# Performance work log

Hardware: AMD Instinct MI355X
Metric: run time of the kernel (lower is better)

Reference implementation:

```python
import jax, jax.numpy as jnp
import numpy as np

DIM = 768
HEADS = 12
HEAD_DIM = DIM // HEADS
HIDDEN = 4 * DIM
B, N = 32, 577
EPS = 1e-5


def _layernorm(x, g, b):
    mu = jnp.mean(x, axis=-1, keepdims=True)
    var = jnp.mean(jnp.square(x - mu), axis=-1, keepdims=True)
    return (x - mu) * jax.lax.rsqrt(var + EPS) * g + b


def setup_inputs() -> dict:
    key = jax.random.key(0)
    ks = jax.random.split(key, 8)
    s = lambda fan_in: 1.0 / np.sqrt(fan_in)
    return {
        "x": jax.random.normal(ks[0], (B, N, DIM), jnp.float32),
        "cp_mask": jax.random.uniform(ks[1], (1, 1, N, N), jnp.float32),
        "ln1_g": jnp.ones((DIM,), jnp.float32),
        "ln1_b": jnp.zeros((DIM,), jnp.float32),
        "w_qkv": jax.random.uniform(ks[2], (DIM, 3 * DIM), jnp.float32, -s(DIM), s(DIM)),
        "w_proj": jax.random.uniform(ks[3], (DIM, DIM), jnp.float32, -s(DIM), s(DIM)),
        "b_proj": jnp.zeros((DIM,), jnp.float32),
        "ln2_g": jnp.ones((DIM,), jnp.float32),
        "ln2_b": jnp.zeros((DIM,), jnp.float32),
        "w_fc1": jax.random.uniform(ks[4], (DIM, HIDDEN), jnp.float32, -s(DIM), s(DIM)),
        "b_fc1": jnp.zeros((HIDDEN,), jnp.float32),
        "w_fc2": jax.random.uniform(ks[5], (HIDDEN, DIM), jnp.float32, -s(HIDDEN), s(HIDDEN)),
        "b_fc2": jnp.zeros((DIM,), jnp.float32),
    }


def reference(x, cp_mask, ln1_g, ln1_b, w_qkv, w_proj, b_proj,
              ln2_g, ln2_b, w_fc1, b_fc1, w_fc2, b_fc2):
    scale = HEAD_DIM ** -0.5
    # --- attention branch ---
    h = _layernorm(x, ln1_g, ln1_b)
    qkv = (h @ w_qkv).reshape(B, N, 3, HEADS, HEAD_DIM)
    q, k, v = jnp.moveaxis(qkv, 2, 0)            # each [B,N,H,Dh]
    q = q.transpose(0, 2, 1, 3)                   # [B,H,N,Dh]
    k = k.transpose(0, 2, 1, 3)
    v = v.transpose(0, 2, 1, 3)
    attn = jnp.einsum('bhnd,bhmd->bhnm', q, k) * scale * cp_mask
    attn = jax.nn.softmax(attn, axis=-1)
    out = jnp.einsum('bhnm,bhmd->bhnd', attn, v)
    out = out.transpose(0, 2, 1, 3).reshape(B, N, DIM)
    out = out @ w_proj + b_proj
    x = x + out
    # --- MLP branch ---
    h = _layernorm(x, ln2_g, ln2_b)
    h = jax.nn.gelu(h @ w_fc1 + b_fc1, approximate=False)
    h = h @ w_fc2 + b_fc2
    return x + h
```

## Files before the change

### kernel.cpp

```cpp
#include <hip/hip_runtime.h>
#include <math.h>

typedef unsigned short u16;
typedef unsigned int u32;
typedef __attribute__((ext_vector_type(8))) short bf16x8;
typedef __attribute__((ext_vector_type(4))) float f32x4;

#define B_    32
#define N_    577
#define DIM_  768
#define HEADS_ 12
#define HD_   64
#define HID_  3072
#define MTOT_ (B_*N_)
#define NP_   640

__device__ __forceinline__ u16 f2b(float f){
  u32 u = __builtin_bit_cast(u32, f);
  u += 0x7fffu + ((u >> 16) & 1u);
  return (u16)(u >> 16);
}
__device__ __forceinline__ u32 cvtpk(float lo, float hi){
  u32 r;
  asm("v_cvt_pk_bf16_f32 %0, %1, %2" : "=v"(r) : "v"(lo), "v"(hi));
  return r;
}

__device__ __forceinline__ void gl_lds16(const void* g, void* l){
  __builtin_amdgcn_global_load_lds(
      (const __attribute__((address_space(1))) u32*)g,
      (__attribute__((address_space(3))) u32*)l, 16, 0, 0);
}
__device__ __forceinline__ void gl_lds4(const void* g, void* l){
  __builtin_amdgcn_global_load_lds(
      (const __attribute__((address_space(1))) u32*)g,
      (__attribute__((address_space(3))) u32*)l, 4, 0, 0);
}

__global__ __launch_bounds__(256) void convT(const float* __restrict__ w,
                                             u16* __restrict__ wt, int K, int N){
  __shared__ float t[32][33];
  int n0 = blockIdx.x * 32, k0 = blockIdx.y * 32;
  int tx = threadIdx.x, ty = threadIdx.y;
  #pragma unroll
  for (int j = 0; j < 4; ++j)
    t[ty + j*8][tx] = w[(size_t)(k0 + ty + j*8) * N + n0 + tx];
  __syncthreads();
  #pragma unroll
  for (int j = 0; j < 4; ++j)
    wt[(size_t)(n0 + ty + j*8) * K + k0 + tx] = f2b(t[tx][ty + j*8]);
}

__global__ __launch_bounds__(256) void ln_k(const float* __restrict__ x,
                                            const float* __restrict__ g,
                                            const float* __restrict__ b,
                                            u16* __restrict__ out){
  int row = blockIdx.x, tid = threadIdx.x;
  const float* xr = x + (size_t)row * DIM_;
  float v0 = xr[tid], v1 = xr[tid + 256], v2 = xr[tid + 512];
  float s = v0 + v1 + v2;
  float s2 = v0*v0 + v1*v1 + v2*v2;
  #pragma unroll
  for (int m = 1; m < 64; m <<= 1){ s += __shfl_xor(s, m); s2 += __shfl_xor(s2, m); }
  __shared__ float ws[8];
  int wid = tid >> 6, ln = tid & 63;
  if (ln == 0){ ws[wid] = s; ws[4 + wid] = s2; }
  __syncthreads();
  s  = ws[0] + ws[1] + ws[2] + ws[3];
  s2 = ws[4] + ws[5] + ws[6] + ws[7];
  float mu = s * (1.0f / DIM_);
  float var = s2 * (1.0f / DIM_) - mu * mu;
  float rs = rsqrtf(var + 1e-5f);
  u16* orow = out + (size_t)row * DIM_;
  orow[tid]       = f2b((v0 - mu) * rs * g[tid]       + b[tid]);
  orow[tid + 256] = f2b((v1 - mu) * rs * g[tid + 256] + b[tid + 256]);
  orow[tid + 512] = f2b((v2 - mu) * rs * g[tid + 512] + b[tid + 512]);
}

#define BM 128
#define BN 128
#define BK 32

template<int EPI>
__global__ __launch_bounds__(256) void gemm_bt(
    const u16* __restrict__ A, const u16* __restrict__ Bt,
    int M, int N, int K,
    const float* __restrict__ bias,
    const float* __restrict__ resid,
    float* __restrict__ outf,
    u16* __restrict__ outb,
    u16* __restrict__ qb, u16* __restrict__ kb, u16* __restrict__ vtb)
{
  __shared__ u16 Al[BM * BK];
  __shared__ u16 Bl[BN * BK];
  int tid = threadIdx.x;
  int wid = tid >> 6, l = tid & 63, ln = l & 15, sub = l >> 4;
  int wm = wid >> 1, wn = wid & 1;

  int nwg  = gridDim.x * gridDim.y;
  int flat = blockIdx.x + gridDim.x * blockIdx.y;
  int q8 = nwg >> 3, r8 = nwg & 7;
  int xcd = flat & 7, j8 = flat >> 3;
  int wgid = (xcd < r8 ? xcd * (q8 + 1) : r8 * (q8 + 1) + (xcd - r8) * q8) + j8;
  int tm = wgid / gridDim.y;
  int tn = wgid - tm * gridDim.y;

  f32x4 acc[4][4] = {};
  int arow = tid >> 2;
  int acol = (tid & 3) * 8;

  int gr0 = tm * BM + arow;      if (gr0 >= M) gr0 = M - 1;
  int gr1 = tm * BM + arow + 64; if (gr1 >= M) gr1 = M - 1;
  const u16* ga0 = A + (size_t)gr0 * K + acol;
  const u16* ga1 = A + (size_t)gr1 * K + acol;
  const u16* gb0 = Bt + (size_t)(tn * BN + arow) * K + acol;
  const u16* gb1 = Bt + (size_t)(tn * BN + arow + 64) * K + acol;
  u16* la0 = &Al[arow * BK + acol];
  u16* la1 = &Al[(arow + 64) * BK + acol];
  u16* lb0 = &Bl[arow * BK + acol];
  u16* lb1 = &Bl[(arow + 64) * BK + acol];

  const int ktiles = K / BK;
  for (int kt = 0; kt < ktiles; ++kt){
    int kbase = kt * BK;
    gl_lds16(ga0 + kbase, la0);
    gl_lds16(ga1 + kbase, la1);
    gl_lds16(gb0 + kbase, lb0);
    gl_lds16(gb1 + kbase, lb1);
    __syncthreads();
    bf16x8 af[4], bfr[4];
    #pragma unroll
    for (int mi = 0; mi < 4; ++mi) af[mi]  = *(const bf16x8*)&Al[(wm*64 + mi*16 + ln) * BK + sub*8];
    #pragma unroll
    for (int ni = 0; ni < 4; ++ni) bfr[ni] = *(const bf16x8*)&Bl[(wn*64 + ni*16 + ln) * BK + sub*8];
    #pragma unroll
    for (int mi = 0; mi < 4; ++mi)
      #pragma unroll
      for (int ni = 0; ni < 4; ++ni)
        acc[mi][ni] = __builtin_amdgcn_mfma_f32_16x16x32_bf16(af[mi], bfr[ni], acc[mi][ni], 0, 0, 0);
    __syncthreads();
  }

  #pragma unroll
  for (int mi = 0; mi < 4; ++mi){
    int rbase = tm * BM + wm * 64 + mi * 16 + sub * 4;
    #pragma unroll
    for (int ni = 0; ni < 4; ++ni){
      int col = tn * BN + wn * 64 + ni * 16 + ln;
      #pragma unroll
      for (int r = 0; r < 4; ++r){
        int grow = rbase + r;
        if (grow >= M) continue;
        float val = acc[mi][ni][r];
        if (EPI == 0){
          u32 bb = (u32)grow / 577u;
          u32 nn = (u32)grow - bb * 577u;
          int which = col / 768;
          int rem = col - which * 768;
          int hh = rem >> 6;
          int d  = col & 63;
          if (which == 0)
            qb[(((size_t)bb * HEADS_ + hh) * N_ + nn) * HD_ + d] = f2b(val);
          else if (which == 1)
            kb[(((size_t)bb * HEADS_ + hh) * N_ + nn) * HD_ + d] = f2b(val);
          else
            vtb[(((size_t)bb * HEADS_ + hh) * HD_ + d) * NP_ + nn] = f2b(val);
        } else if (EPI == 1){
          outf[(size_t)grow * N + col] = val + bias[col] + resid[(size_t)grow * N + col];
        } else {
          float t = val + bias[col];
          float ge = 0.5f * t * (1.0f + erff(t * 0.70710678118654752f));
          outb[(size_t)grow * N + col] = f2b(ge);
        }
      }
    }
  }
}

__global__ __launch_bounds__(256) void attn_k(
    const u16* __restrict__ q, const u16* __restrict__ k,
    const u16* __restrict__ vt, const float* __restrict__ mask,
    u16* __restrict__ o)
{
  const float SCALE = 0.125f;
  int bh = blockIdx.x, qt = blockIdx.y;
  int tid = threadIdx.x;
  int wid = tid >> 6, l = tid & 63, ln = l & 15, sub = l >> 4;
  int b = bh / HEADS_, hh = bh - b * HEADS_;
  int qrow0_blk = qt * 64;
  int qrow0 = qrow0_blk + wid * 16;

  __shared__ u16 Kl[64 * 64];
  __shared__ u16 Vl[64 * 64];
  __shared__ float Ml[64 * 64];
  __shared__ u16 Pl[4][16 * 64];

  int qr = qrow0 + ln; if (qr > N_ - 1) qr = N_ - 1;
  const u16* qbase = q + ((size_t)bh * N_ + qr) * HD_;
  bf16x8 qf0 = *(const bf16x8*)&qbase[sub * 8];
  bf16x8 qf1 = *(const bf16x8*)&qbase[32 + sub * 8];

  f32x4 oacc[4] = {};
  float mrun = -1e30f, lrun = 0.f;

  for (int mt = 0; mt < 10; ++mt){
    int mbase = mt * 64;
    #pragma unroll
    for (int p = 0; p < 2; ++p){
      int row = (tid >> 3) + p * 32;
      int sc = (tid & 7) ^ (row & 7);
      int kr = mbase + row; if (kr > N_ - 1) kr = N_ - 1;
      gl_lds16(&k[((size_t)bh * N_ + kr) * HD_ + sc * 8], &Kl[row * 64 + (tid & 7) * 8]);
      gl_lds16(&vt[((size_t)bh * HD_ + row) * NP_ + mbase + sc * 8], &Vl[row * 64 + (tid & 7) * 8]);
    }
    if (mbase + 63 < N_){
      #pragma unroll
      for (int p = 0; p < 4; ++p){
        int row = (tid >> 4) + p * 16;
        int grow = qrow0_blk + row; if (grow > N_ - 1) grow = N_ - 1;
        int sc = (tid & 15) ^ (row & 15);
        gl_lds16(&mask[(size_t)grow * N_ + mbase + sc * 4], &Ml[row * 64 + (tid & 15) * 4]);
      }
    } else {
      #pragma unroll
      for (int p = 0; p < 16; ++p){
        int row = (tid >> 6) + p * 4;
        int grow = qrow0_blk + row; if (grow > N_ - 1) grow = N_ - 1;
        int kp = tid & 63;
        int lcol = ((((kp >> 2) ^ (row & 15)) << 2) | (kp & 3));
        int gcol = mbase + lcol; if (gcol > N_ - 1) gcol = N_ - 1;
        gl_lds4(&mask[(size_t)grow * N_ + gcol], &Ml[row * 64 + kp]);
      }
    }
    __syncthreads();

    f32x4 s[4];
    #pragma unroll
    for (int c = 0; c < 4; ++c){
      int krow = c * 16 + ln;
      bf16x8 kf0 = *(const bf16x8*)&Kl[krow * 64 + ((sub    ) ^ (krow & 7)) * 8];
      bf16x8 kf1 = *(const bf16x8*)&Kl[krow * 64 + ((4 + sub) ^ (krow & 7)) * 8];
      f32x4 z = {};
      z = __builtin_amdgcn_mfma_f32_16x16x32_bf16(kf0, qf0, z, 0, 0, 0);
      z = __builtin_amdgcn_mfma_f32_16x16x32_bf16(kf1, qf1, z, 0, 0, 0);
      s[c] = z;
    }
    int mrow = wid * 16 + ln;
    #pragma unroll
    for (int c = 0; c < 4; ++c){
      f32x4 mv = *(const f32x4*)&Ml[mrow * 64 + (((c * 4 + sub) ^ ln) << 2)];
      int mg0 = mbase + c * 16 + sub * 4;
      #pragma unroll
      for (int r = 0; r < 4; ++r){
        if (mg0 + r < N_) s[c][r] = s[c][r] * SCALE * mv[r];
        else              s[c][r] = -1e30f;
      }
    }
    float pm = s[0][0];
    #pragma unroll
    for (int c = 0; c < 4; ++c)
      #pragma unroll
      for (int r = 0; r < 4; ++r) pm = fmaxf(pm, s[c][r]);
    pm = fmaxf(pm, __shfl_xor(pm, 16));
    pm = fmaxf(pm, __shfl_xor(pm, 32));
    float mnew = fmaxf(mrun, pm);
    float alpha = __expf(mrun - mnew);
    mrun = mnew;
    float ps = 0.f;
    #pragma unroll
    for (int c = 0; c < 4; ++c)
      #pragma unroll
      for (int r = 0; r < 4; ++r){
        float p = __expf(s[c][r] - mrun);
        s[c][r] = p;
        ps += p;
      }
    ps += __shfl_xor(ps, 16);
    ps += __shfl_xor(ps, 32);
    lrun = lrun * alpha + ps;
    #pragma unroll
    for (int c = 0; c < 4; ++c)
      #pragma unroll
      for (int h = 0; h < 2; ++h){
        int kk = c * 16 + sub * 4 + 2 * h;
        u32 w = cvtpk(s[c][2 * h], s[c][2 * h + 1]);
        *(u32*)&Pl[wid][ln * 64 + (((kk >> 3) ^ (ln & 7)) << 3) + (kk & 7)] = w;
      }
    float a_d[4];
    #pragma unroll
    for (int r = 0; r < 4; ++r) a_d[r] = __shfl(alpha, sub * 4 + r);
    #pragma unroll
    for (int dt = 0; dt < 4; ++dt)
      #pragma unroll
      for (int r = 0; r < 4; ++r) oacc[dt][r] *= a_d[r];
    #pragma unroll
    for (int kbv = 0; kbv < 2; ++kbv){
      bf16x8 pa = *(const bf16x8*)&Pl[wid][ln * 64 + (((kbv * 4 + sub) ^ (ln & 7)) << 3)];
      #pragma unroll
      for (int dt = 0; dt < 4; ++dt){
        int vrow = dt * 16 + ln;
        bf16x8 vf = *(const bf16x8*)&Vl[vrow * 64 + (((kbv * 4 + sub) ^ (vrow & 7)) << 3)];
        oacc[dt] = __builtin_amdgcn_mfma_f32_16x16x32_bf16(pa, vf, oacc[dt], 0, 0, 0);
      }
    }
    __syncthreads();
  }
  float rinv = 1.0f / lrun;
  float inv_d[4];
  #pragma unroll
  for (int r = 0; r < 4; ++r) inv_d[r] = __shfl(rinv, sub * 4 + r);
  #pragma unroll
  for (int dt = 0; dt < 4; ++dt)
    #pragma unroll
    for (int r = 0; r < 4; ++r){
      int qg = qrow0 + sub * 4 + r;
      if (qg < N_)
        o[((size_t)b * N_ + qg) * DIM_ + hh * HD_ + dt * 16 + ln] = f2b(oacc[dt][r] * inv_d[r]);
    }
}

#define OFF_WQKV  0ull
#define OFF_WPROJ 3538944ull
#define OFF_WFC1  4718592ull
#define OFF_WFC2  9437184ull
#define OFF_BUFA  14155776ull
#define OFF_BUFB  (OFF_BUFA + 28360704ull)
#define OFF_BUFC  (OFF_BUFB + 28360704ull)
#define OFF_VT    (OFF_BUFC + 28360704ull)

extern "C" void kernel_launch(void* const* d_in, const int* in_sizes, int n_in,
                              void* d_out, int out_size, void* d_ws, size_t ws_size,
                              hipStream_t stream)
{
  const float* x     = (const float*)d_in[0];
  const float* mask  = (const float*)d_in[1];
  const float* ln1g  = (const float*)d_in[2];
  const float* ln1b  = (const float*)d_in[3];
  const float* wqkv  = (const float*)d_in[4];
  const float* wproj = (const float*)d_in[5];
  const float* bproj = (const float*)d_in[6];
  const float* ln2g  = (const float*)d_in[7];
  const float* ln2b  = (const float*)d_in[8];
  const float* wfc1  = (const float*)d_in[9];
  const float* bfc1  = (const float*)d_in[10];
  const float* wfc2  = (const float*)d_in[11];
  const float* bfc2  = (const float*)d_in[12];
  float* out = (float*)d_out;

  char* ws = (char*)d_ws;
  u16* wqkv_t  = (u16*)(ws + OFF_WQKV);
  u16* wproj_t = (u16*)(ws + OFF_WPROJ);
  u16* wfc1_t  = (u16*)(ws + OFF_WFC1);
  u16* wfc2_t  = (u16*)(ws + OFF_WFC2);
  u16* hbuf  = (u16*)(ws + OFF_BUFA);
  u16* obuf  = (u16*)(ws + OFF_BUFA);
  u16* qbuf  = (u16*)(ws + OFF_BUFB);
  u16* h2buf = (u16*)(ws + OFF_BUFB);
  u16* kbuf  = (u16*)(ws + OFF_BUFC);
  u16* vtbuf = (u16*)(ws + OFF_VT);
  u16* h3buf = (u16*)(ws + OFF_BUFC);

  dim3 tb(32, 8);
  convT<<<dim3(2304/32, 768/32), tb, 0, stream>>>(wqkv,  wqkv_t,  768,  2304);
  convT<<<dim3(768/32,  768/32), tb, 0, stream>>>(wproj, wproj_t, 768,  768);
  convT<<<dim3(3072/32, 768/32), tb, 0, stream>>>(wfc1,  wfc1_t,  768,  3072);
  convT<<<dim3(768/32, 3072/32), tb, 0, stream>>>(wfc2,  wfc2_t,  3072, 768);

  ln_k<<<MTOT_, 256, 0, stream>>>(x, ln1g, ln1b, hbuf);

  gemm_bt<0><<<dim3(145, 18), 256, 0, stream>>>(hbuf, wqkv_t, MTOT_, 2304, 768,
      nullptr, nullptr, nullptr, nullptr, qbuf, kbuf, vtbuf);

  attn_k<<<dim3(384, 10), 256, 0, stream>>>(qbuf, kbuf, vtbuf, mask, obuf);

  gemm_bt<1><<<dim3(145, 6), 256, 0, stream>>>(obuf, wproj_t, MTOT_, 768, 768,
      bproj, x, out, nullptr, nullptr, nullptr, nullptr);

  ln_k<<<MTOT_, 256, 0, stream>>>(out, ln2g, ln2b, h2buf);

  const int M0 = 9216, M1 = MTOT_ - M0;
  gemm_bt<2><<<dim3(72, 24), 256, 0, stream>>>(h2buf, wfc1_t, M0, 3072, 768,
      bfc1, nullptr, nullptr, h3buf, nullptr, nullptr, nullptr);
  gemm_bt<1><<<dim3(72, 6), 256, 0, stream>>>(h3buf, wfc2_t, M0, 768, 3072,
      bfc2, out, out, nullptr, nullptr, nullptr, nullptr);
  gemm_bt<2><<<dim3(73, 24), 256, 0, stream>>>(h2buf + (size_t)M0 * 768, wfc1_t, M1, 3072, 768,
      bfc1, nullptr, nullptr, h3buf, nullptr, nullptr, nullptr);
  gemm_bt<1><<<dim3(73, 6), 256, 0, stream>>>(h3buf, wfc2_t, M1, 768, 3072,
      bfc2, out + (size_t)M0 * 768, out + (size_t)M0 * 768, nullptr, nullptr, nullptr, nullptr);
}
```

Measured before the change: 908.0 us.

## Double-buffer LDS tiles in GEMM to overlap global loads with MFMA

The GEMM kernel now keeps two LDS buffers for the A and B tiles. It preloads the first k-tile, then issues the direct-to-LDS loads for the next k-tile before running the MFMAs on the current one. This hides global-memory latency behind compute and removes one barrier per k-iteration. In exchange, LDS use per workgroup doubles, which may lower occupancy.

Result: faster. 868.1 us (-4.4%).

```diff
diff --git a/kernel.cpp b/kernel.cpp
--- a/kernel.cpp
+++ b/kernel.cpp
@@ -91,8 +91,8 @@
     u16* __restrict__ outb,
     u16* __restrict__ qb, u16* __restrict__ kb, u16* __restrict__ vtb)
 {
-  __shared__ u16 Al[BM * BK];
-  __shared__ u16 Bl[BN * BK];
+  __shared__ u16 Al[2][BM * BK];
+  __shared__ u16 Bl[2][BN * BK];
   int tid = threadIdx.x;
   int wid = tid >> 6, l = tid & 63, ln = l & 15, sub = l >> 4;
   int wm = wid >> 1, wn = wid & 1;
@@ -115,30 +115,38 @@
   const u16* ga1 = A + (size_t)gr1 * K + acol;
   const u16* gb0 = Bt + (size_t)(tn * BN + arow) * K + acol;
   const u16* gb1 = Bt + (size_t)(tn * BN + arow + 64) * K + acol;
-  u16* la0 = &Al[arow * BK + acol];
-  u16* la1 = &Al[(arow + 64) * BK + acol];
-  u16* lb0 = &Bl[arow * BK + acol];
-  u16* lb1 = &Bl[(arow + 64) * BK + acol];
+  int s0 = arow * BK + acol;
+  int s1 = (arow + 64) * BK + acol;
 
   const int ktiles = K / BK;
+  gl_lds16(ga0, &Al[0][s0]);
+  gl_lds16(ga1, &Al[0][s1]);
+  gl_lds16(gb0, &Bl[0][s0]);
+  gl_lds16(gb1, &Bl[0][s1]);
+  __syncthreads();
+
+  int cur = 0;
   for (int kt = 0; kt < ktiles; ++kt){
-    int kbase = kt * BK;
-    gl_lds16(ga0 + kbase, la0);
-    gl_lds16(ga1 + kbase, la1);
-    gl_lds16(gb0 + kbase, lb0);
-    gl_lds16(gb1 + kbase, lb1);
-    __syncthreads();
+    int nxt = cur ^ 1;
+    if (kt + 1 < ktiles){
+      int kb = (kt + 1) * BK;
+      gl_lds16(ga0 + kb, &Al[nxt][s0]);
+      gl_lds16(ga1 + kb, &Al[nxt][s1]);
+      gl_lds16(gb0 + kb, &Bl[nxt][s0]);
+      gl_lds16(gb1 + kb, &Bl[nxt][s1]);
+    }
     bf16x8 af[4], bfr[4];
     #pragma unroll
-    for (int mi = 0; mi < 4; ++mi) af[mi]  = *(const bf16x8*)&Al[(wm*64 + mi*16 + ln) * BK + sub*8];
-    #pragma unroll
-    for (int ni = 0; ni < 4; ++ni) bfr[ni] = *(const bf16x8*)&Bl[(wn*64 + ni*16 + ln) * BK + sub*8];
+    for (int mi = 0; mi < 4; ++mi) af[mi]  = *(const bf16x8*)&Al[cur][(wm*64 + mi*16 + ln) * BK + sub*8];
+    #pragma unroll
+    for (int ni = 0; ni < 4; ++ni) bfr[ni] = *(const bf16x8*)&Bl[cur][(wn*64 + ni*16 + ln) * BK + sub*8];
     #pragma unroll
     for (int mi = 0; mi < 4; ++mi)
       #pragma unroll
       for (int ni = 0; ni < 4; ++ni)
         acc[mi][ni] = __builtin_amdgcn_mfma_f32_16x16x32_bf16(af[mi], bfr[ni], acc[mi][ni], 0, 0, 0);
     __syncthreads();
+    cur = nxt;
   }
 
   #pragma unroll
```

## Triple-buffer GEMM LDS tiles with async prefetch and XOR-swizzled layout

Applied to the files above, without the earlier changes.

Converts the GEMM main loop to a three-stage LDS ring buffer. Global-to-LDS loads are issued two tiles ahead, and explicit vmcnt waits plus a single barrier per iteration replace the two syncthreads. It also XOR-swizzles the k-column chunk by row, so fragment reads from LDS avoid bank conflicts. This uses three times the LDS per block, which may reduce occupancy, and it relies on careful waitcnt accounting for correctness.

Measured after the change: 869.3 us. 4.3% less time.

```diff
diff --git a/kernel.cpp b/kernel.cpp
--- a/kernel.cpp
+++ b/kernel.cpp
@@ -91,8 +91,8 @@
     u16* __restrict__ outb,
     u16* __restrict__ qb, u16* __restrict__ kb, u16* __restrict__ vtb)
 {
-  __shared__ u16 Al[BM * BK];
-  __shared__ u16 Bl[BN * BK];
+  __shared__ u16 Al[3][BM * BK];
+  __shared__ u16 Bl[3][BN * BK];
   int tid = threadIdx.x;
   int wid = tid >> 6, l = tid & 63, ln = l & 15, sub = l >> 4;
   int wm = wid >> 1, wn = wid & 1;
@@ -107,38 +107,53 @@
 
   f32x4 acc[4][4] = {};
   int arow = tid >> 2;
-  int acol = (tid & 3) * 8;
+  int t4   = tid & 3;
+  int scol = (t4 ^ ((arow >> 1) & 3)) * 8;
 
   int gr0 = tm * BM + arow;      if (gr0 >= M) gr0 = M - 1;
   int gr1 = tm * BM + arow + 64; if (gr1 >= M) gr1 = M - 1;
-  const u16* ga0 = A + (size_t)gr0 * K + acol;
-  const u16* ga1 = A + (size_t)gr1 * K + acol;
-  const u16* gb0 = Bt + (size_t)(tn * BN + arow) * K + acol;
-  const u16* gb1 = Bt + (size_t)(tn * BN + arow + 64) * K + acol;
-  u16* la0 = &Al[arow * BK + acol];
-  u16* la1 = &Al[(arow + 64) * BK + acol];
-  u16* lb0 = &Bl[arow * BK + acol];
-  u16* lb1 = &Bl[(arow + 64) * BK + acol];
+  const u16* ga0 = A + (size_t)gr0 * K + scol;
+  const u16* ga1 = A + (size_t)gr1 * K + scol;
+  const u16* gb0 = Bt + (size_t)(tn * BN + arow) * K + scol;
+  const u16* gb1 = Bt + (size_t)(tn * BN + arow + 64) * K + scol;
+  int s0 = arow * BK + t4 * 8;
+  int s1 = (arow + 64) * BK + t4 * 8;
+  int csw = (sub ^ ((ln >> 1) & 3)) * 8;
 
   const int ktiles = K / BK;
+  gl_lds16(ga0,      &Al[0][s0]);
+  gl_lds16(ga1,      &Al[0][s1]);
+  gl_lds16(gb0,      &Bl[0][s0]);
+  gl_lds16(gb1,      &Bl[0][s1]);
+  gl_lds16(ga0 + BK, &Al[1][s0]);
+  gl_lds16(ga1 + BK, &Al[1][s1]);
+  gl_lds16(gb0 + BK, &Bl[1][s0]);
+  gl_lds16(gb1 + BK, &Bl[1][s1]);
+
   for (int kt = 0; kt < ktiles; ++kt){
-    int kbase = kt * BK;
-    gl_lds16(ga0 + kbase, la0);
-    gl_lds16(ga1 + kbase, la1);
-    gl_lds16(gb0 + kbase, lb0);
-    gl_lds16(gb1 + kbase, lb1);
-    __syncthreads();
+    if (kt + 1 < ktiles) asm volatile("s_waitcnt vmcnt(4)" ::: "memory");
+    else                 asm volatile("s_waitcnt vmcnt(0)" ::: "memory");
+    __builtin_amdgcn_s_barrier();
+    if (kt + 2 < ktiles){
+      int bnx = (kt + 2) % 3;
+      int kb = (kt + 2) * BK;
+      gl_lds16(ga0 + kb, &Al[bnx][s0]);
+      gl_lds16(ga1 + kb, &Al[bnx][s1]);
+      gl_lds16(gb0 + kb, &Bl[bnx][s0]);
+      gl_lds16(gb1 + kb, &Bl[bnx][s1]);
+    }
+    const u16* Ac = Al[kt % 3];
+    const u16* Bc = Bl[kt % 3];
     bf16x8 af[4], bfr[4];
     #pragma unroll
-    for (int mi = 0; mi < 4; ++mi) af[mi]  = *(const bf16x8*)&Al[(wm*64 + mi*16 + ln) * BK + sub*8];
-    #pragma unroll
-    for (int ni = 0; ni < 4; ++ni) bfr[ni] = *(const bf16x8*)&Bl[(wn*64 + ni*16 + ln) * BK + sub*8];
+    for (int mi = 0; mi < 4; ++mi) af[mi]  = *(const bf16x8*)&Ac[(wm*64 + mi*16 + ln) * BK + csw];
+    #pragma unroll
+    for (int ni = 0; ni < 4; ++ni) bfr[ni] = *(const bf16x8*)&Bc[(wn*64 + ni*16 + ln) * BK + csw];
     #pragma unroll
     for (int mi = 0; mi < 4; ++mi)
       #pragma unroll
       for (int ni = 0; ni < 4; ++ni)
         acc[mi][ni] = __builtin_amdgcn_mfma_f32_16x16x32_bf16(af[mi], bfr[ni], acc[mi][ni], 0, 0, 0);
-    __syncthreads();
   }
 
   #pragma unroll
```
